# Kernel tuning notes

Hardware: AMD Instinct MI355X
Metric: run time of the kernel (lower is better)

Reference implementation:

```python
import jax, jax.numpy as jnp
import numpy as np
from jax import lax

HIDDEN = 50


def setup_inputs() -> dict:
    key = jax.random.key(0)
    ks = jax.random.split(key, 8)
    B, T, I, H, O = 8192, 256, 1, HIDDEN, 1
    s = 0.1  # small init scale, keeps tanh/sigmoid in a sane range
    return {
        "x": jax.random.normal(ks[0], (B, T, I), dtype=jnp.float32),
        "W_ih": jax.random.normal(ks[1], (4 * H, I), dtype=jnp.float32) * s,
        "W_hh": jax.random.normal(ks[2], (4 * H, H), dtype=jnp.float32) * s,
        "b_ih": jax.random.normal(ks[3], (4 * H,), dtype=jnp.float32) * s,
        "b_hh": jax.random.normal(ks[4], (4 * H,), dtype=jnp.float32) * s,
        "W_lin": jax.random.normal(ks[5], (O, H), dtype=jnp.float32) * s,
        "b_lin": jax.random.normal(ks[6], (O,), dtype=jnp.float32) * s,
    }


def reference(x, W_ih, W_hh, b_ih, b_hh, W_lin, b_lin):
    # Single-layer batch_first LSTM; PyTorch gate order is (i, f, g, o).
    # lstm_out[:, -1] == final hidden state h_T for num_layers=1, so we only
    # carry (h, c) and never materialize the full [B, T, H] output.
    # Dropout is identity in eval mode.
    B = x.shape[0]
    b = b_ih + b_hh  # [4H]

    def step(carry, x_t):
        h, c = carry  # [B, H] each
        gates = x_t @ W_ih.T + h @ W_hh.T + b  # [B, 4H]
        i, f, g, o = jnp.split(gates, 4, axis=-1)
        i = jax.nn.sigmoid(i)
        f = jax.nn.sigmoid(f)
        g = jnp.tanh(g)
        o = jax.nn.sigmoid(o)
        c = f * c + i * g
        h = o * jnp.tanh(c)
        return (h, c), None

    xs = jnp.swapaxes(x, 0, 1)  # [T, B, I]
    h0 = jnp.zeros((B, HIDDEN), dtype=x.dtype)
    (hT, _), _ = lax.scan(step, (h0, h0), xs)
    return hT @ W_lin.T + b_lin  # [B, output_size]
```

## Files before the change

### kernel.cpp

```cpp
#include <hip/hip_runtime.h>


#define NTH 896
#define TST 256
#define MB 16
#define NBLK 512
#define HR 72
#define HSZ (MB * HR)

#define LOG2E 1.44269504088896f

typedef __attribute__((ext_vector_type(8))) _Float16 half8;
typedef __attribute__((ext_vector_type(4))) float float4v;

__device__ __forceinline__ float rcp_(float v)  { return __builtin_amdgcn_rcpf(v); }
__device__ __forceinline__ float exp2_(float v) { return __builtin_amdgcn_exp2f(v); }
__device__ __forceinline__ unsigned short f16bits(float v) {
    _Float16 h = (_Float16)v;
    return *(unsigned short*)&h;
}

__global__ __launch_bounds__(NTH, 7) void lstm_mfma(
    const float* __restrict__ x,
    const float* __restrict__ W_ih,
    const float* __restrict__ W_hh,
    const float* __restrict__ b_ih,
    const float* __restrict__ b_hh,
    const float* __restrict__ W_lin,
    const float* __restrict__ b_lin,
    float* __restrict__ out)
{
    __shared__ __align__(16) unsigned short Hh[2 * HSZ];

    const int tid  = threadIdx.x;
    const int wv   = tid >> 6;
    const int ln   = tid & 63;
    const int lrow = ln & 15;
    const int quad = ln >> 4;
    const int bbase = (int)blockIdx.x * MB;
    const int T = wv;

    half8 wh[2], wl[2];
    {
        const int gr = T * 16 + lrow;
        const int j  = gr >> 2, g = gr & 3;
        const int row = g * 50 + j;
        const float scl = (g == 2) ? (2.0f * LOG2E) : (-LOG2E);
        #pragma unroll
        for (int q2 = 0; q2 < 2; ++q2) {
            half8 h8, l8;
            #pragma unroll
            for (int i = 0; i < 8; ++i) {
                const int k = q2 * 32 + quad * 8 + i;
                float V = 0.0f;
                if (j < 50) {
                    if (k < 50)       V = W_hh[row * 50 + k];
                    else if (k == 50) V = W_ih[row];
                    else if (k == 51) V = b_ih[row] + b_hh[row];
                }
                V *= scl;
                _Float16 hi = (_Float16)V;
                h8[i] = hi;
                l8[i] = (_Float16)(V - (float)hi);
            }
            wh[q2] = h8;
            wl[q2] = l8;
        }
    }

    for (int i = tid; i < HSZ; i += NTH)
        ((unsigned int*)Hh)[i] = 0u;
    __syncthreads();
    if (tid < MB) {
        float xv = x[(bbase + tid) * TST + 0];
        Hh[tid * HR + 50] = f16bits(xv);
        Hh[tid * HR + 51] = 0x3C00;
        Hh[HSZ + tid * HR + 51] = 0x3C00;
    }
    __syncthreads();

    float c = 0.0f;
    const unsigned short* Hr = &Hh[lrow * HR + quad * 8];
    int jw = T * 4 + quad;
    if (jw >= 50) jw = 52 + quad;
    unsigned short* Hw = &Hh[lrow * HR + jw];
    const float* xr = &x[(bbase + lrow) * TST];
    const float4v z4 = {0.f, 0.f, 0.f, 0.f};

    auto step1 = [&](int roff, int woff) {
        const half8 b0 = *(const half8*)(Hr + roff);
        const half8 b1 = *(const half8*)(Hr + roff + 32);

        float4v a4;
        a4 = __builtin_amdgcn_mfma_f32_16x16x32_f16(wh[0], b0, z4, 0, 0, 0);
        a4 = __builtin_amdgcn_mfma_f32_16x16x32_f16(wh[1], b1, a4, 0, 0, 0);
        a4 = __builtin_amdgcn_mfma_f32_16x16x32_f16(wl[0], b0, a4, 0, 0, 0);
        a4 = __builtin_amdgcn_mfma_f32_16x16x32_f16(wl[1], b1, a4, 0, 0, 0);

        float i_ = rcp_(1.0f + exp2_(a4[0]));
        float f_ = rcp_(1.0f + exp2_(a4[1]));
        float g_ = fmaf(-2.0f, rcp_(exp2_(a4[2]) + 1.0f), 1.0f);
        float o_ = rcp_(1.0f + exp2_(a4[3]));
        float cn = f_ * c + i_ * g_;
        c = cn;
        float th = fmaf(-2.0f, rcp_(exp2_(2.0f * LOG2E * cn) + 1.0f), 1.0f);
        float hn = o_ * th;

        Hw[woff] = f16bits(hn);
    };

    #pragma unroll 1
    for (int t2 = 0; t2 < TST / 2; ++t2) {
        if (wv == 13) {
            const float xA = xr[2 * t2 + 1];
            const float xB = xr[(2 * t2 + 2) & 255];
            if (ln < 16)
                Hh[HSZ + lrow * HR + 50] = f16bits(xA);
            __syncthreads();
            if (ln < 16)
                Hh[lrow * HR + 50] = f16bits(xB);
            __syncthreads();
        } else {
            step1(0, HSZ);
            __syncthreads();
            step1(HSZ, 0);
            __syncthreads();
        }
    }

    if (tid < MB) {
        float s = b_lin[0];
        #pragma unroll 10
        for (int k = 0; k < 50; ++k) {
            float hk = (float)(*(const _Float16*)&Hh[tid * HR + k]);
            s += hk * W_lin[k];
        }
        out[bbase + tid] = s;
    }
}

extern "C" void kernel_launch(void* const* d_in, const int* in_sizes, int n_in,
                              void* d_out, int out_size, void* d_ws, size_t ws_size,
                              hipStream_t stream) {
    const float* x     = (const float*)d_in[0];
    const float* W_ih  = (const float*)d_in[1];
    const float* W_hh  = (const float*)d_in[2];
    const float* b_ih  = (const float*)d_in[3];
    const float* b_hh  = (const float*)d_in[4];
    const float* W_lin = (const float*)d_in[5];
    const float* b_lin = (const float*)d_in[6];
    float* out = (float*)d_out;

    lstm_mfma<<<dim3(NBLK), dim3(NTH), 0, stream>>>(
        x, W_ih, W_hh, b_ih, b_hh, W_lin, b_lin, out);
}
```

Baseline: 225.7 us.

## Pack two gate tiles per wave and shrink block to eight waves

Reduces the block from 14 to 8 waves by having six waves compute two 16-row gate tiles each (one wave computes one, one loads x). The goal is to cut barrier participants and expose instruction-level parallelism between two independent MFMA chains per wave. The cost is a longer serial per-step path per wave and more registers for the doubled weight fragments.

```diff
diff --git a/kernel.cpp b/kernel.cpp
--- a/kernel.cpp
+++ b/kernel.cpp
@@ -1,7 +1,7 @@
 #include <hip/hip_runtime.h>
 
 
-#define NTH 896
+#define NTH 512
 #define TST 256
 #define MB 16
 #define NBLK 512
@@ -20,7 +20,7 @@
     return *(unsigned short*)&h;
 }
 
-__global__ __launch_bounds__(NTH, 7) void lstm_mfma(
+__global__ __launch_bounds__(NTH, 8) void lstm_mfma(
     const float* __restrict__ x,
     const float* __restrict__ W_ih,
     const float* __restrict__ W_hh,
@@ -38,10 +38,12 @@
     const int lrow = ln & 15;
     const int quad = ln >> 4;
     const int bbase = (int)blockIdx.x * MB;
-    const int T = wv;
 
-    half8 wh[2], wl[2];
-    {
+    half8 wh[2][2], wl[2][2];
+    #pragma unroll
+    for (int s = 0; s < 2; ++s) {
+        const int T  = wv + 7 * s;
+        const bool tval = (wv < 7) && (T <= 12);
         const int gr = T * 16 + lrow;
         const int j  = gr >> 2, g = gr & 3;
         const int row = g * 50 + j;
@@ -53,7 +55,7 @@
             for (int i = 0; i < 8; ++i) {
                 const int k = q2 * 32 + quad * 8 + i;
                 float V = 0.0f;
-                if (j < 50) {
+                if (tval && j < 50) {
                     if (k < 50)       V = W_hh[row * 50 + k];
                     else if (k == 50) V = W_ih[row];
                     else if (k == 51) V = b_ih[row] + b_hh[row];
@@ -63,8 +65,8 @@
                 h8[i] = hi;
                 l8[i] = (_Float16)(V - (float)hi);
             }
-            wh[q2] = h8;
-            wl[q2] = l8;
+            wh[s][q2] = h8;
+            wl[s][q2] = l8;
         }
     }
 
@@ -79,39 +81,58 @@
     }
     __syncthreads();
 
-    float c = 0.0f;
+    float c0 = 0.0f, c1 = 0.0f;
     const unsigned short* Hr = &Hh[lrow * HR + quad * 8];
-    int jw = T * 4 + quad;
-    if (jw >= 50) jw = 52 + quad;
-    unsigned short* Hw = &Hh[lrow * HR + jw];
+    int jw0 = wv * 4 + quad;       if (jw0 >= 50) jw0 = 52 + quad;
+    int jw1 = (wv + 7) * 4 + quad; if (jw1 >= 50) jw1 = 52 + quad;
+    unsigned short* Hw0 = &Hh[lrow * HR + jw0];
+    unsigned short* Hw1 = &Hh[lrow * HR + jw1];
     const float* xr = &x[(bbase + lrow) * TST];
     const float4v z4 = {0.f, 0.f, 0.f, 0.f};
+    const bool two_tiles = (wv < 6);
 
     auto step1 = [&](int roff, int woff) {
         const half8 b0 = *(const half8*)(Hr + roff);
         const half8 b1 = *(const half8*)(Hr + roff + 32);
 
         float4v a4;
-        a4 = __builtin_amdgcn_mfma_f32_16x16x32_f16(wh[0], b0, z4, 0, 0, 0);
-        a4 = __builtin_amdgcn_mfma_f32_16x16x32_f16(wh[1], b1, a4, 0, 0, 0);
-        a4 = __builtin_amdgcn_mfma_f32_16x16x32_f16(wl[0], b0, a4, 0, 0, 0);
-        a4 = __builtin_amdgcn_mfma_f32_16x16x32_f16(wl[1], b1, a4, 0, 0, 0);
+        a4 = __builtin_amdgcn_mfma_f32_16x16x32_f16(wh[0][0], b0, z4, 0, 0, 0);
+        a4 = __builtin_amdgcn_mfma_f32_16x16x32_f16(wh[0][1], b1, a4, 0, 0, 0);
+        a4 = __builtin_amdgcn_mfma_f32_16x16x32_f16(wl[0][0], b0, a4, 0, 0, 0);
+        a4 = __builtin_amdgcn_mfma_f32_16x16x32_f16(wl[0][1], b1, a4, 0, 0, 0);
+        float4v a5 = z4;
+        if (two_tiles) {
+            a5 = __builtin_amdgcn_mfma_f32_16x16x32_f16(wh[1][0], b0, z4, 0, 0, 0);
+            a5 = __builtin_amdgcn_mfma_f32_16x16x32_f16(wh[1][1], b1, a5, 0, 0, 0);
+            a5 = __builtin_amdgcn_mfma_f32_16x16x32_f16(wl[1][0], b0, a5, 0, 0, 0);
+            a5 = __builtin_amdgcn_mfma_f32_16x16x32_f16(wl[1][1], b1, a5, 0, 0, 0);
+        }
 
-        float i_ = rcp_(1.0f + exp2_(a4[0]));
-        float f_ = rcp_(1.0f + exp2_(a4[1]));
-        float g_ = fmaf(-2.0f, rcp_(exp2_(a4[2]) + 1.0f), 1.0f);
-        float o_ = rcp_(1.0f + exp2_(a4[3]));
-        float cn = f_ * c + i_ * g_;
-        c = cn;
-        float th = fmaf(-2.0f, rcp_(exp2_(2.0f * LOG2E * cn) + 1.0f), 1.0f);
-        float hn = o_ * th;
-
-        Hw[woff] = f16bits(hn);
+        {
+            float i_ = rcp_(1.0f + exp2_(a4[0]));
+            float f_ = rcp_(1.0f + exp2_(a4[1]));
+            float g_ = fmaf(-2.0f, rcp_(exp2_(a4[2]) + 1.0f), 1.0f);
+            float o_ = rcp_(1.0f + exp2_(a4[3]));
+            float cn = f_ * c0 + i_ * g_;
+            c0 = cn;
+            float th = fmaf(-2.0f, rcp_(exp2_(2.0f * LOG2E * cn) + 1.0f), 1.0f);
+            Hw0[woff] = f16bits(o_ * th);
+        }
+        if (two_tiles) {
+            float i_ = rcp_(1.0f + exp2_(a5[0]));
+            float f_ = rcp_(1.0f + exp2_(a5[1]));
+            float g_ = fmaf(-2.0f, rcp_(exp2_(a5[2]) + 1.0f), 1.0f);
+            float o_ = rcp_(1.0f + exp2_(a5[3]));
+            float cn = f_ * c1 + i_ * g_;
+            c1 = cn;
+            float th = fmaf(-2.0f, rcp_(exp2_(2.0f * LOG2E * cn) + 1.0f), 1.0f);
+            Hw1[woff] = f16bits(o_ * th);
+        }
     };
 
     #pragma unroll 1
     for (int t2 = 0; t2 < TST / 2; ++t2) {
-        if (wv == 13) {
+        if (wv == 7) {
             const float xA = xr[2 * t2 + 1];
             const float xB = xr[(2 * t2 + 2) & 255];
             if (ln < 16)
```

After: 247.0 us. +9.4%, slower.
